# Kernel optimization log

Hardware: AMD Instinct MI355X
Metric: run time of the kernel (lower is better)

## Reference

```python
import jax, jax.numpy as jnp
import numpy as np
from jax import lax

STRIDE, PAD, K = 1, 1, 3


def conv2d(x, w, b, stride, pad):
    y = lax.conv_general_dilated(x, w, (stride, stride), [(pad, pad), (pad, pad)],
                                 dimension_numbers=('NCHW', 'OIHW', 'NCHW'))
    return y + b[None, :, None, None]


def deform_conv2d(x, offset, mask, weight, stride, pad):
    # torchvision DeformConv2d v2 (modulated): offset channels are (dy, dx) pairs per tap.
    B, C, H, W = x.shape
    O = weight.shape[0]
    K2 = K * K
    Ho = (H + 2 * pad - K) // stride + 1
    Wo = (W + 2 * pad - K) // stride + 1
    off = offset.reshape(B, K2, 2, Ho, Wo)
    dy, dx = off[:, :, 0], off[:, :, 1]                      # [B,K2,Ho,Wo]
    ki = (jnp.arange(K2) // K).astype(x.dtype)[None, :, None, None]
    kj = (jnp.arange(K2) % K).astype(x.dtype)[None, :, None, None]
    hg = (jnp.arange(Ho) * stride - pad).astype(x.dtype)[None, None, :, None]
    wg = (jnp.arange(Wo) * stride - pad).astype(x.dtype)[None, None, None, :]
    py = hg + ki + dy                                        # sampling y coord [B,K2,Ho,Wo]
    px = wg + kj + dx
    y0 = jnp.floor(py)
    x0 = jnp.floor(px)
    ly = py - y0
    lx = px - x0
    y0i = y0.astype(jnp.int32)
    x0i = x0.astype(jnp.int32)
    x_flat = x.reshape(B, C, H * W)

    def gather(iy, ix):
        valid = ((iy >= 0) & (iy < H) & (ix >= 0) & (ix < W)).astype(x.dtype)
        idx = jnp.clip(iy, 0, H - 1) * W + jnp.clip(ix, 0, W - 1)   # [B,K2,Ho,Wo]
        v = jax.vmap(lambda xf, id_: xf[:, id_])(x_flat, idx)       # [B,C,K2,Ho,Wo]
        return v * valid[:, None]

    v = ((1 - ly) * (1 - lx))[:, None] * gather(y0i, x0i) \
      + ((1 - ly) * lx)[:, None] * gather(y0i, x0i + 1) \
      + (ly * (1 - lx))[:, None] * gather(y0i + 1, x0i) \
      + (ly * lx)[:, None] * gather(y0i + 1, x0i + 1)
    v = v * mask[:, None]                                    # modulate per tap
    return jnp.einsum('bckhw,ock->bohw', v, weight.reshape(O, C, K2))


def setup_inputs():
    key = jax.random.key(0)
    ks = jax.random.split(key, 5)
    B, C, H, W, O = 4, 64, 96, 96, 128
    x = jax.random.normal(ks[0], (B, C, H, W), jnp.float32)
    offset_w = jax.random.normal(ks[1], (2 * K * K, C, K, K), jnp.float32) * 0.01
    offset_b = jax.random.normal(ks[2], (2 * K * K,), jnp.float32) * 0.1
    mod_w = jax.random.normal(ks[3], (K * K, C, K, K), jnp.float32) * 0.01
    mod_b = jnp.zeros((K * K,), jnp.float32)
    deform_w = jax.random.normal(ks[4], (O, C, K, K), jnp.float32) * (1.0 / np.sqrt(C * K * K))
    return {"x": x, "offset_w": offset_w, "offset_b": offset_b,
            "mod_w": mod_w, "mod_b": mod_b, "deform_w": deform_w}


def reference(x, offset_w, offset_b, mod_w, mod_b, deform_w):
    offset = conv2d(x, offset_w, offset_b, STRIDE, PAD)
    modulator = 2.0 * jax.nn.sigmoid(conv2d(x, mod_w, mod_b, STRIDE, PAD))
    return deform_conv2d(x, offset, modulator, deform_w, STRIDE, PAD)
```

## Files before the change

kernel.cpp:

```cpp
#include <hip/hip_runtime.h>
#include <math.h>

#define Bc 4
#define Cc 64
#define Hh 96
#define Ww 96
#define Oo 128
#define HW 9216
#define PT 32
#define NPB 288
#define RW 34
#define RS 72

typedef __attribute__((ext_vector_type(8))) short bf16x8;
typedef __attribute__((ext_vector_type(4))) float f32x4;

__device__ inline unsigned short f2bf(float f) {
    unsigned u = __builtin_bit_cast(unsigned, f);
    return (unsigned short)((u + 0x7FFF + ((u >> 16) & 1)) >> 16);
}
__device__ inline float bf2f(short s) {
    return __builtin_bit_cast(float, ((unsigned)(unsigned short)s) << 16);
}

__global__ __launch_bounds__(256) void k_pre(
    const float* __restrict__ dw, const float* __restrict__ ow,
    const float* __restrict__ mw, const float* __restrict__ x,
    unsigned short* __restrict__ wTmF, unsigned short* __restrict__ w27F,
    unsigned short* __restrict__ xT)
{
    const int bid = blockIdx.x;
    const int t = threadIdx.x;
    if (bid < 360) {
        int i = bid * 256 + t;
        if (i < 9 * 8 * 2 * 512) {
            int j = i & 7, l = (i >> 3) & 63, fb = i >> 9;
            int s = fb & 1, m = (fb >> 1) & 7, k = fb >> 4;
            int oc = m * 16 + (l & 15);
            int c = s * 32 + (l >> 4) * 8 + j;
            wTmF[i] = f2bf(dw[(oc * 64 + c) * 9 + k]);
        }
        int jj = i - 9 * 8 * 2 * 512;
        if (jj >= 0 && jj < 9 * 2 * 2 * 512) {
            int j = jj & 7, l = (jj >> 3) & 63, fb2 = jj >> 9;
            int nt = fb2 & 1, s = (fb2 >> 1) & 1, k = fb2 >> 2;
            int ch = nt * 16 + (l & 15);
            int c = s * 32 + (l >> 4) * 8 + j;
            float v = 0.f;
            if (ch < 18)      v = ow[(ch * 64 + c) * 9 + k];
            else if (ch < 27) v = mw[((ch - 18) * 64 + c) * 9 + k];
            w27F[jj] = f2bf(v);
        }
    } else {
        int gp = (bid - 360) * 256 + t;
        int b = gp / HW;
        int p = gp - b * HW;
        const float* xb = x + (size_t)b * Cc * HW + p;
        unsigned short* op = xT + (size_t)gp * 64;
#pragma unroll
        for (int q = 0; q < 8; ++q) {
            union { bf16x8 v8; unsigned short us[8]; } u;
#pragma unroll
            for (int c = 0; c < 8; ++c)
                u.us[c] = f2bf(xb[(size_t)(q * 8 + c) * HW]);
            *(bf16x8*)(op + q * 8) = u.v8;
        }
    }
}

template <int K0, int K1>
__device__ __forceinline__ void sample_gemm(
    const unsigned short* __restrict__ xTb,
    const unsigned short* __restrict__ wb,
    const float (&pw)[9][4][PT], const int (&pi)[9][4][PT],
    int pos_l, int cq, f32x4 (&acc)[8])
{
    constexpr int NH = 2 * (K1 - K0);
    bf16x8 buf[3][4];

    auto issue = [&](int hs) {
        const int kk = K0 + (hs >> 1), so = (hs & 1) * 32;
#pragma unroll
        for (int cr = 0; cr < 4; ++cr)
            buf[hs % 3][cr] =
                *(const bf16x8*)(xTb + pi[kk][cr][pos_l] + so + cq);
    };

    issue(0);
    issue(1);

#pragma unroll
    for (int hs = 0; hs < NH; ++hs) {
        if (hs + 2 < NH) issue(hs + 2);
        const int kk = K0 + (hs >> 1), s = hs & 1;
        const float w0 = pw[kk][0][pos_l], w1 = pw[kk][1][pos_l];
        const float w2 = pw[kk][2][pos_l], w3 = pw[kk][3][pos_l];
        union { bf16x8 v8; unsigned short us[8]; } B;
#pragma unroll
        for (int j = 0; j < 8; ++j)
            B.us[j] = f2bf(w0 * bf2f(buf[hs % 3][0][j])
                         + w1 * bf2f(buf[hs % 3][1][j])
                         + w2 * bf2f(buf[hs % 3][2][j])
                         + w3 * bf2f(buf[hs % 3][3][j]));
#pragma unroll
        for (int m = 0; m < 8; ++m) {
            bf16x8 A = *(const bf16x8*)(wb + (size_t)((kk * 16 + m * 2 + s) << 9));
            acc[m] = __builtin_amdgcn_mfma_f32_16x16x32_bf16(A, B.v8, acc[m], 0, 0, 0);
        }
    }
}

__global__ __launch_bounds__(256, 4) void k_fused(
    const unsigned short* __restrict__ xT, const float* __restrict__ ob,
    const float* __restrict__ mb, const unsigned short* __restrict__ w27F,
    const unsigned short* __restrict__ wTmF, float* __restrict__ out)
{
    __shared__ union Ovl {
        short xreg[3 * RW * RS];
        struct {
            float pw[9][4][PT];
            int   pi[9][4][PT];
        } p;
        float mg[8 * 520];
    } ovl;
    __shared__ float offm_s[27 * 33];

    const int t = threadIdx.x;
    const int lid = (blockIdx.x & 7) * 144 + (blockIdx.x >> 3);
    const int bb = lid / NPB;
    const int tile = lid - bb * NPB;
    const int ho = tile / 3;
    const int wo0 = (tile - ho * 3) * 32;
    const int wv = t >> 6;
    const int l = t & 63;
    const int lr = l & 15;
    const int quad = l >> 4;

    const unsigned short* xTb = xT + (size_t)bb * HW * 64;

    static const bf16x8 zero8 = {0, 0, 0, 0, 0, 0, 0, 0};
    for (int i = t; i < 3 * RW * 8; i += 256) {
        int q = i & 7;
        int rc = i >> 3;
        int col = rc % RW, r = rc / RW;
        int h = ho + r - 1, w = wo0 + col - 1;
        bf16x8 val = zero8;
        if ((unsigned)h < (unsigned)Hh && (unsigned)w < (unsigned)Ww)
            val = *(const bf16x8*)(xTb + ((size_t)(h * Ww + w)) * 64 + q * 8);
        *(bf16x8*)&ovl.xreg[(r * RW + col) * RS + q * 8] = val;
    }
    __syncthreads();

    {
        f32x4 acc_o = {0.f, 0.f, 0.f, 0.f};
        const int mt1 = wv & 1;
        const int nt1 = wv >> 1;
#pragma unroll
        for (int k9 = 0; k9 < 9; ++k9) {
            const int di = k9 / 3, dj = k9 % 3;
            const short* ar = &ovl.xreg[(di * RW + mt1 * 16 + lr + dj) * RS + quad * 8];
#pragma unroll
            for (int s = 0; s < 2; ++s) {
                bf16x8 a = *(const bf16x8*)(ar + s * 32);
                bf16x8 b = *(const bf16x8*)(w27F + (((k9 * 2 + s) * 2 + nt1) << 9) + l * 8);
                acc_o = __builtin_amdgcn_mfma_f32_16x16x32_bf16(a, b, acc_o, 0, 0, 0);
            }
        }
        __syncthreads();
        int ch = nt1 * 16 + lr;
        if (ch < 27) {
#pragma unroll
            for (int r = 0; r < 4; ++r)
                offm_s[ch * 33 + mt1 * 16 + quad * 4 + r] = acc_o[r];
        }
    }
    __syncthreads();

    for (int i = t; i < 27 * PT; i += 256) {
        int ch = i >> 5, pos = i & 31;
        float v = offm_s[ch * 33 + pos];
        if (ch < 18) v += ob[ch];
        else         v = 2.f / (1.f + expf(-(v + mb[ch - 18])));
        offm_s[ch * 33 + pos] = v;
    }
    __syncthreads();
    for (int i = t; i < 9 * PT; i += 256) {
        int kk = i >> 5, pos = i & 31;
        float dy = offm_s[(2 * kk) * 33 + pos];
        float dx = offm_s[(2 * kk + 1) * 33 + pos];
        float mm = offm_s[(18 + kk) * 33 + pos];
        float py = (float)(ho - 1 + kk / 3) + dy;
        float px = (float)(wo0 + pos - 1 + kk % 3) + dx;
        float fy = floorf(py), fx = floorf(px);
        float ly = py - fy, lx = px - fx;
        int y0 = (int)fy, x0 = (int)fx;
        int y1 = y0 + 1, x1 = x0 + 1;
        float v00 = ((unsigned)y0 < (unsigned)Hh && (unsigned)x0 < (unsigned)Ww) ? 1.f : 0.f;
        float v01 = ((unsigned)y0 < (unsigned)Hh && (unsigned)x1 < (unsigned)Ww) ? 1.f : 0.f;
        float v10 = ((unsigned)y1 < (unsigned)Hh && (unsigned)x0 < (unsigned)Ww) ? 1.f : 0.f;
        float v11 = ((unsigned)y1 < (unsigned)Hh && (unsigned)x1 < (unsigned)Ww) ? 1.f : 0.f;
        int cy0 = min(max(y0, 0), Hh - 1), cy1 = min(max(y1, 0), Hh - 1);
        int cx0 = min(max(x0, 0), Ww - 1), cx1 = min(max(x1, 0), Ww - 1);
        ovl.p.pw[kk][0][pos] = (1.f - ly) * (1.f - lx) * mm * v00;
        ovl.p.pw[kk][1][pos] = (1.f - ly) * lx * mm * v01;
        ovl.p.pw[kk][2][pos] = ly * (1.f - lx) * mm * v10;
        ovl.p.pw[kk][3][pos] = ly * lx * mm * v11;
        ovl.p.pi[kk][0][pos] = (cy0 * Ww + cx0) * 64;
        ovl.p.pi[kk][1][pos] = (cy0 * Ww + cx1) * 64;
        ovl.p.pi[kk][2][pos] = (cy1 * Ww + cx0) * 64;
        ovl.p.pi[kk][3][pos] = (cy1 * Ww + cx1) * 64;
    }
    __syncthreads();

    const int nt = wv & 1;
    const int tg = wv >> 1;
    const int pos_l = nt * 16 + lr;
    const int cq = quad * 8;

    f32x4 acc[8];
#pragma unroll
    for (int m = 0; m < 8; ++m) acc[m] = (f32x4){0.f, 0.f, 0.f, 0.f};

    const unsigned short* wb = wTmF + l * 8;

    if (tg == 0)
        sample_gemm<0, 5>(xTb, wb, ovl.p.pw, ovl.p.pi, pos_l, cq, acc);
    else
        sample_gemm<5, 9>(xTb, wb, ovl.p.pw, ovl.p.pi, pos_l, cq, acc);

    __syncthreads();
    if (tg == 1) {
#pragma unroll
        for (int m = 0; m < 8; ++m)
            *(f32x4*)&ovl.mg[m * 520 + (nt * 64 + l) * 4] = acc[m];
    }
    __syncthreads();
    if (tg == 0) {
        float* outp = out + (size_t)bb * Oo * HW + tile * PT + nt * 16 + lr;
#pragma unroll
        for (int m = 0; m < 8; ++m) {
            f32x4 o = acc[m] + *(const f32x4*)&ovl.mg[m * 520 + (nt * 64 + l) * 4];
#pragma unroll
            for (int r = 0; r < 4; ++r) {
                int oc = m * 16 + quad * 4 + r;
                outp[(size_t)oc * HW] = o[r];
            }
        }
    }
}

extern "C" void kernel_launch(void* const* d_in, const int* in_sizes, int n_in,
                              void* d_out, int out_size, void* d_ws, size_t ws_size,
                              hipStream_t stream) {
    const float* x  = (const float*)d_in[0];
    const float* ow = (const float*)d_in[1];
    const float* ob = (const float*)d_in[2];
    const float* mw = (const float*)d_in[3];
    const float* mb = (const float*)d_in[4];
    const float* dw = (const float*)d_in[5];
    float* out = (float*)d_out;

    unsigned short* wTmF = (unsigned short*)d_ws;
    unsigned short* w27F = wTmF + 9 * 8 * 2 * 512;
    unsigned short* xT   = w27F + 9 * 2 * 2 * 512;

    hipLaunchKernelGGL(k_pre, dim3(504), dim3(256), 0, stream,
                       dw, ow, mw, x, wTmF, w27F, xT);
    hipLaunchKernelGGL(k_fused, dim3(Bc * NPB), dim3(256), 0, stream,
                       xT, ob, mb, w27F, wTmF, out);
}
```

Baseline: 117.6 us.

## Stage a wider input halo in LDS and sample deformable taps from it

The LDS input tile grows from a 3x34 to a 7x38 pixel halo. The bilinear sampling phase now reads corner pixels from shared memory when they fall inside this halo and falls back to global loads, using a sign-bit flag in the index, only for out-of-tile samples. A wave-wide ballot selects a fast path that does only LDS reads. This is meant to replace scattered global gathers with LDS reads, since the small offsets keep most samples near the output. In exchange it uses much more shared memory, which drops the occupancy hint from 4 to 3 blocks, removes the register-pipelined prefetch of global loads, and adds a larger tile-load phase.

```diff
diff --git a/kernel.cpp b/kernel.cpp
--- a/kernel.cpp
+++ b/kernel.cpp
@@ -9,7 +9,8 @@
 #define HW 9216
 #define PT 32
 #define NPB 288
-#define RW 34
+#define RR 7
+#define RC 38
 #define RS 72
 
 typedef __attribute__((ext_vector_type(8))) short bf16x8;
@@ -70,59 +71,64 @@
 
 template <int K0, int K1>
 __device__ __forceinline__ void sample_gemm(
+    const short (&reg)[RR * RC * RS],
     const unsigned short* __restrict__ xTb,
     const unsigned short* __restrict__ wb,
     const float (&pw)[9][4][PT], const int (&pi)[9][4][PT],
     int pos_l, int cq, f32x4 (&acc)[8])
 {
-    constexpr int NH = 2 * (K1 - K0);
-    bf16x8 buf[3][4];
-
-    auto issue = [&](int hs) {
-        const int kk = K0 + (hs >> 1), so = (hs & 1) * 32;
-#pragma unroll
-        for (int cr = 0; cr < 4; ++cr)
-            buf[hs % 3][cr] =
-                *(const bf16x8*)(xTb + pi[kk][cr][pos_l] + so + cq);
-    };
-
-    issue(0);
-    issue(1);
-
-#pragma unroll
-    for (int hs = 0; hs < NH; ++hs) {
-        if (hs + 2 < NH) issue(hs + 2);
-        const int kk = K0 + (hs >> 1), s = hs & 1;
+#pragma unroll
+    for (int kk = K0; kk < K1; ++kk) {
         const float w0 = pw[kk][0][pos_l], w1 = pw[kk][1][pos_l];
         const float w2 = pw[kk][2][pos_l], w3 = pw[kk][3][pos_l];
-        union { bf16x8 v8; unsigned short us[8]; } B;
-#pragma unroll
-        for (int j = 0; j < 8; ++j)
-            B.us[j] = f2bf(w0 * bf2f(buf[hs % 3][0][j])
-                         + w1 * bf2f(buf[hs % 3][1][j])
-                         + w2 * bf2f(buf[hs % 3][2][j])
-                         + w3 * bf2f(buf[hs % 3][3][j]));
-#pragma unroll
-        for (int m = 0; m < 8; ++m) {
-            bf16x8 A = *(const bf16x8*)(wb + (size_t)((kk * 16 + m * 2 + s) << 9));
-            acc[m] = __builtin_amdgcn_mfma_f32_16x16x32_bf16(A, B.v8, acc[m], 0, 0, 0);
-        }
-    }
-}
-
-__global__ __launch_bounds__(256, 4) void k_fused(
+        const int i0 = pi[kk][0][pos_l], i1 = pi[kk][1][pos_l];
+        const int i2 = pi[kk][2][pos_l], i3 = pi[kk][3][pos_l];
+        const unsigned long long anybad = __ballot((i0 | i1 | i2 | i3) < 0);
+
+#pragma unroll
+        for (int s = 0; s < 2; ++s) {
+            const int so = s * 32 + cq;
+            bf16x8 c0, c1, c2, c3;
+            if (anybad == 0) {
+                c0 = *(const bf16x8*)(&reg[i0 + so]);
+                c1 = *(const bf16x8*)(&reg[i1 + so]);
+                c2 = *(const bf16x8*)(&reg[i2 + so]);
+                c3 = *(const bf16x8*)(&reg[i3 + so]);
+            } else {
+                c0 = (i0 < 0) ? *(const bf16x8*)(xTb + (i0 & 0x7FFFFFFF) + so)
+                              : *(const bf16x8*)(&reg[i0 + so]);
+                c1 = (i1 < 0) ? *(const bf16x8*)(xTb + (i1 & 0x7FFFFFFF) + so)
+                              : *(const bf16x8*)(&reg[i1 + so]);
+                c2 = (i2 < 0) ? *(const bf16x8*)(xTb + (i2 & 0x7FFFFFFF) + so)
+                              : *(const bf16x8*)(&reg[i2 + so]);
+                c3 = (i3 < 0) ? *(const bf16x8*)(xTb + (i3 & 0x7FFFFFFF) + so)
+                              : *(const bf16x8*)(&reg[i3 + so]);
+            }
+            union { bf16x8 v8; unsigned short us[8]; } B;
+#pragma unroll
+            for (int j = 0; j < 8; ++j)
+                B.us[j] = f2bf(w0 * bf2f(c0[j]) + w1 * bf2f(c1[j])
+                             + w2 * bf2f(c2[j]) + w3 * bf2f(c3[j]));
+#pragma unroll
+            for (int m = 0; m < 8; ++m) {
+                bf16x8 A = *(const bf16x8*)(wb + (size_t)((kk * 16 + m * 2 + s) << 9));
+                acc[m] = __builtin_amdgcn_mfma_f32_16x16x32_bf16(A, B.v8, acc[m], 0, 0, 0);
+            }
+        }
+    }
+}
+
+__global__ __launch_bounds__(256, 3) void k_fused(
     const unsigned short* __restrict__ xT, const float* __restrict__ ob,
     const float* __restrict__ mb, const unsigned short* __restrict__ w27F,
     const unsigned short* __restrict__ wTmF, float* __restrict__ out)
 {
-    __shared__ union Ovl {
-        short xreg[3 * RW * RS];
-        struct {
-            float pw[9][4][PT];
-            int   pi[9][4][PT];
-        } p;
+    __shared__ union RU {
+        short reg[RR * RC * RS];
         float mg[8 * 520];
-    } ovl;
+    } R;
+    __shared__ float s_pw[9][4][PT];
+    __shared__ int   s_pi[9][4][PT];
     __shared__ float offm_s[27 * 33];
 
     const int t = threadIdx.x;
@@ -139,15 +145,15 @@
     const unsigned short* xTb = xT + (size_t)bb * HW * 64;
 
     static const bf16x8 zero8 = {0, 0, 0, 0, 0, 0, 0, 0};
-    for (int i = t; i < 3 * RW * 8; i += 256) {
+    for (int i = t; i < RR * RC * 8; i += 256) {
         int q = i & 7;
-        int rc = i >> 3;
-        int col = rc % RW, r = rc / RW;
-        int h = ho + r - 1, w = wo0 + col - 1;
+        int rcx = i >> 3;
+        int col = rcx % RC, r = rcx / RC;
+        int h = ho - 3 + r, w = wo0 - 3 + col;
         bf16x8 val = zero8;
         if ((unsigned)h < (unsigned)Hh && (unsigned)w < (unsigned)Ww)
             val = *(const bf16x8*)(xTb + ((size_t)(h * Ww + w)) * 64 + q * 8);
-        *(bf16x8*)&ovl.xreg[(r * RW + col) * RS + q * 8] = val;
+        *(bf16x8*)&R.reg[(r * RC + col) * RS + q * 8] = val;
     }
     __syncthreads();
 
@@ -158,7 +164,8 @@
 #pragma unroll
         for (int k9 = 0; k9 < 9; ++k9) {
             const int di = k9 / 3, dj = k9 % 3;
-            const short* ar = &ovl.xreg[(di * RW + mt1 * 16 + lr + dj) * RS + quad * 8];
+            const short* ar =
+                &R.reg[((di + 2) * RC + mt1 * 16 + lr + dj + 2) * RS + quad * 8];
 #pragma unroll
             for (int s = 0; s < 2; ++s) {
                 bf16x8 a = *(const bf16x8*)(ar + s * 32);
@@ -166,7 +173,6 @@
                 acc_o = __builtin_amdgcn_mfma_f32_16x16x32_bf16(a, b, acc_o, 0, 0, 0);
             }
         }
-        __syncthreads();
         int ch = nt1 * 16 + lr;
         if (ch < 27) {
 #pragma unroll
@@ -199,16 +205,22 @@
         float v01 = ((unsigned)y0 < (unsigned)Hh && (unsigned)x1 < (unsigned)Ww) ? 1.f : 0.f;
         float v10 = ((unsigned)y1 < (unsigned)Hh && (unsigned)x0 < (unsigned)Ww) ? 1.f : 0.f;
         float v11 = ((unsigned)y1 < (unsigned)Hh && (unsigned)x1 < (unsigned)Ww) ? 1.f : 0.f;
-        int cy0 = min(max(y0, 0), Hh - 1), cy1 = min(max(y1, 0), Hh - 1);
-        int cx0 = min(max(x0, 0), Ww - 1), cx1 = min(max(x1, 0), Ww - 1);
-        ovl.p.pw[kk][0][pos] = (1.f - ly) * (1.f - lx) * mm * v00;
-        ovl.p.pw[kk][1][pos] = (1.f - ly) * lx * mm * v01;
-        ovl.p.pw[kk][2][pos] = ly * (1.f - lx) * mm * v10;
-        ovl.p.pw[kk][3][pos] = ly * lx * mm * v11;
-        ovl.p.pi[kk][0][pos] = (cy0 * Ww + cx0) * 64;
-        ovl.p.pi[kk][1][pos] = (cy0 * Ww + cx1) * 64;
-        ovl.p.pi[kk][2][pos] = (cy1 * Ww + cx0) * 64;
-        ovl.p.pi[kk][3][pos] = (cy1 * Ww + cx1) * 64;
+        s_pw[kk][0][pos] = (1.f - ly) * (1.f - lx) * mm * v00;
+        s_pw[kk][1][pos] = (1.f - ly) * lx * mm * v01;
+        s_pw[kk][2][pos] = ly * (1.f - lx) * mm * v10;
+        s_pw[kk][3][pos] = ly * lx * mm * v11;
+
+        auto mkidx = [&](float valid, int y, int xx) -> int {
+            if (valid == 0.f) return 0;
+            int ry = y - (ho - 3), rx = xx - (wo0 - 3);
+            if ((unsigned)ry < (unsigned)RR && (unsigned)rx < (unsigned)RC)
+                return (ry * RC + rx) * RS;
+            return (int)(0x80000000u | (unsigned)((y * Ww + xx) * 64));
+        };
+        s_pi[kk][0][pos] = mkidx(v00, y0, x0);
+        s_pi[kk][1][pos] = mkidx(v01, y0, x1);
+        s_pi[kk][2][pos] = mkidx(v10, y1, x0);
+        s_pi[kk][3][pos] = mkidx(v11, y1, x1);
     }
     __syncthreads();
 
@@ -224,22 +236,22 @@
     const unsigned short* wb = wTmF + l * 8;
 
     if (tg == 0)
-        sample_gemm<0, 5>(xTb, wb, ovl.p.pw, ovl.p.pi, pos_l, cq, acc);
+        sample_gemm<0, 5>(R.reg, xTb, wb, s_pw, s_pi, pos_l, cq, acc);
     else
-        sample_gemm<5, 9>(xTb, wb, ovl.p.pw, ovl.p.pi, pos_l, cq, acc);
+        sample_gemm<5, 9>(R.reg, xTb, wb, s_pw, s_pi, pos_l, cq, acc);
 
     __syncthreads();
     if (tg == 1) {
 #pragma unroll
         for (int m = 0; m < 8; ++m)
-            *(f32x4*)&ovl.mg[m * 520 + (nt * 64 + l) * 4] = acc[m];
+            *(f32x4*)&R.mg[m * 520 + (nt * 64 + l) * 4] = acc[m];
     }
     __syncthreads();
     if (tg == 0) {
         float* outp = out + (size_t)bb * Oo * HW + tile * PT + nt * 16 + lr;
 #pragma unroll
         for (int m = 0; m < 8; ++m) {
-            f32x4 o = acc[m] + *(const f32x4*)&ovl.mg[m * 520 + (nt * 64 + l) * 4];
+            f32x4 o = acc[m] + *(const f32x4*)&R.mg[m * 520 + (nt * 64 + l) * 4];
 #pragma unroll
             for (int r = 0; r < 4; ++r) {
                 int oc = m * 16 + quad * 4 + r;
```

Result: faster. 106.7 us (-9.3%).
